# Kernel optimization log

Hardware: AMD Instinct MI355X
Metric: run time of the kernel (lower is better)

The kernel has to match this reference:

```python
import jax, jax.numpy as jnp
import numpy as np

NUM_LEVELS = 4  # -> num_components = 4*5/2 = 10 (non-recursive weights)


def _excl_cumsum(x, axis):
    # exclusive cumulative sum along `axis` (forward direction)
    return jnp.cumsum(x, axis=axis) - x


def setup_inputs() -> dict:
    key = jax.random.key(0)
    k1, k2, k3 = jax.random.split(key, 3)
    B, T, F, m = 32, 2048, 128, 64
    C = NUM_LEVELS * (NUM_LEVELS + 1) // 2  # 10
    X = jax.random.normal(k1, (B, T, F), dtype=jnp.float32)
    kernel = jax.random.normal(k2, (C, F, m), dtype=jnp.float32) / np.sqrt(F)
    bias = jax.random.normal(k3, (C, m), dtype=jnp.float32) * 0.01
    return {"X": X, "kernel": kernel, "bias": bias}


def reference(X, kernel, bias):
    # low_rank_seq2tens, embedding_order=1, recursive_weights=False,
    # reverse=False, return_sequences=False
    # M: [C, B, T, m] -- low-rank projections of the sequence for each component
    M = jnp.einsum('btf,cfm->cbtm', X, kernel) + bias[:, None, None, :]
    Y = [jnp.sum(M[0], axis=1)]  # level 1: plain time-sum, [B, m]
    k = 1
    for i in range(1, NUM_LEVELS):
        R = M[k]
        k += 1
        for _ in range(1, i + 1):
            # iterated-sum recurrence: multiply by next component's projection of
            # the exclusive prefix sum along time
            R = M[k] * _excl_cumsum(R, axis=1)
            k += 1
        Y.append(jnp.sum(R, axis=1))
    return jnp.stack(Y, axis=1)  # [B, num_levels, m]
```

## Files before the change

### kernel.cpp

```cpp
#include <hip/hip_runtime.h>
#include <hip/hip_bf16.h>
#include <stdint.h>


typedef __attribute__((ext_vector_type(8))) short short8;
typedef __attribute__((ext_vector_type(4))) float f32x4;

#define T_ 2048
#define F_ 128
#define M_ 64
#define NTILE 40
#define SEGS 16

__device__ __forceinline__ unsigned short f2bf(float x){
  unsigned int u = __float_as_uint(x);
  u += 0x7FFFu + ((u>>16)&1u);
  return (unsigned short)(u>>16);
}
__device__ __forceinline__ float bf2f(unsigned short s){
  return __uint_as_float(((unsigned int)s)<<16);
}

__global__ __launch_bounds__(256) void prep_w_k(const float* __restrict__ Wk,
                                                uint4* __restrict__ wsw){
  int g = blockIdx.x*256 + threadIdx.x;
  if (g >= NTILE*4*64) return;
  int l  = g & 63;
  int kk = (g >> 6) & 3;
  int n  = g >> 8;
  int cm = n*16 + (l & 15);
  int c  = cm >> 6, mm = cm & 63;
  int kb = kk*32 + (l>>4)*8;
  unsigned short v[8];
  #pragma unroll
  for (int j=0;j<8;++j) v[j] = f2bf(Wk[((c*F_) + kb + j)*M_ + mm]);
  uint4 o;
  o.x = (unsigned)v[0] | ((unsigned)v[1]<<16);
  o.y = (unsigned)v[2] | ((unsigned)v[3]<<16);
  o.z = (unsigned)v[4] | ((unsigned)v[5]<<16);
  o.w = (unsigned)v[6] | ((unsigned)v[7]<<16);
  wsw[g] = o;
}

struct Q4 { uint2 q0,q1,q2,q3; };

__global__ __launch_bounds__(128) void ls2t_main_k(const float* __restrict__ X,
                                                   const float* __restrict__ bias,
                                                   const short8* __restrict__ wfrag,
                                                   float* __restrict__ agg){
  const int chunk = blockIdx.x;
  const int b     = blockIdx.y;
  const int tid = threadIdx.x;
  const int w  = tid >> 6;
  const int l  = tid & 63;
  const int lr = l & 15, lg = l >> 4;
  const int t0 = chunk*128 + w*64;

  __shared__ char lds_raw[65536];
  char* msb = lds_raw + w*32768;

  short8 afr[4][4];
  #pragma unroll
  for (int s=0;s<4;++s){
    const float* xrow = X + ((size_t)b*T_ + t0 + s*16 + lr)*F_ + lg*8;
    #pragma unroll
    for (int kk=0;kk<4;++kk){
      float4 x0 = *reinterpret_cast<const float4*>(xrow + kk*32);
      float4 x1 = *reinterpret_cast<const float4*>(xrow + kk*32 + 4);
      short8 a;
      a[0]=(short)f2bf(x0.x); a[1]=(short)f2bf(x0.y);
      a[2]=(short)f2bf(x0.z); a[3]=(short)f2bf(x0.w);
      a[4]=(short)f2bf(x1.x); a[5]=(short)f2bf(x1.y);
      a[6]=(short)f2bf(x1.z); a[7]=(short)f2bf(x1.w);
      afr[s][kk]=a;
    }
  }

  auto comp = [&](int c, int ci){
    short8 wfr[4][4];
    #pragma unroll
    for (int nt=0;nt<4;++nt)
      #pragma unroll
      for (int kk=0;kk<4;++kk)
        wfr[nt][kk] = wfrag[((c*4+nt)*4+kk)*64 + l];
    #pragma unroll
    for (int nt=0;nt<4;++nt){
      #pragma unroll
      for (int s=0;s<4;++s){
        f32x4 acc = {0.f,0.f,0.f,0.f};
        #pragma unroll
        for (int kk=0;kk<4;++kk)
          acc = __builtin_amdgcn_mfma_f32_16x16x32_bf16(afr[s][kk], wfr[nt][kk], acc, 0,0,0);
        unsigned lo = (unsigned)f2bf(acc[0]) | ((unsigned)f2bf(acc[1])<<16);
        unsigned hi = (unsigned)f2bf(acc[2]) | ((unsigned)f2bf(acc[3])<<16);
        *reinterpret_cast<uint2*>(msb + ci*8192 + s*2048 + (nt*16+lr)*32 + ((lg^nt)&3)*8)
            = make_uint2(lo, hi);
      }
    }
  };
  auto rdq = [&](int ci, int s)->Q4{
    Q4 r;
    r.q0 = *reinterpret_cast<const uint2*>(msb + ci*8192 + s*2048 + l*32 + ((0^lg)&3)*8);
    r.q1 = *reinterpret_cast<const uint2*>(msb + ci*8192 + s*2048 + l*32 + ((1^lg)&3)*8);
    r.q2 = *reinterpret_cast<const uint2*>(msb + ci*8192 + s*2048 + l*32 + ((2^lg)&3)*8);
    r.q3 = *reinterpret_cast<const uint2*>(msb + ci*8192 + s*2048 + l*32 + ((3^lg)&3)*8);
    return r;
  };

#define EXTV(rq, j) bf2f((unsigned short)(((j)&1)?((((j)&2)?(rq).y:(rq).x)>>16):((((j)&2)?(rq).y:(rq).x)&0xffffu)))
#define PICKQ(r, q) ((q)==0?(r).q0:(q)==1?(r).q1:(q)==2?(r).q2:(r).q3)

  float S0=0;
  {
    float bz0 = bias[0*64+l];
    comp(0,0);
    #pragma unroll
    for (int s=0;s<4;++s){
      Q4 r0 = rdq(0,s);
      #pragma unroll
      for (int q=0;q<4;++q){
        uint2 rq = PICKQ(r0,q);
        #pragma unroll
        for (int j=0;j<4;++j) S0 += EXTV(rq,j) + bz0;
      }
    }
  }
  float S1=0,S2=0,I21=0;
  {
    float bz1=bias[64+l], bz2=bias[128+l];
    comp(1,0); comp(2,1);
    float p1=0;
    #pragma unroll
    for (int s=0;s<4;++s){
      Q4 r1 = rdq(0,s), r2 = rdq(1,s);
      #pragma unroll
      for (int q=0;q<4;++q){
        uint2 a1q = PICKQ(r1,q), a2q = PICKQ(r2,q);
        #pragma unroll
        for (int j=0;j<4;++j){
          float a1 = EXTV(a1q,j)+bz1;
          float a2 = EXTV(a2q,j)+bz2;
          I21 += a2*p1; p1 += a1; S1 += a1; S2 += a2;
        }
      }
    }
  }
  float S3=0,S4=0,S5=0,I43=0,I54=0,I543=0;
  {
    float bz3=bias[192+l], bz4=bias[256+l], bz5=bias[320+l];
    comp(3,0); comp(4,1); comp(5,2);
    float p3=0,p4=0,p43=0;
    #pragma unroll
    for (int s=0;s<4;++s){
      Q4 r3 = rdq(0,s), r4 = rdq(1,s), r5 = rdq(2,s);
      #pragma unroll
      for (int q=0;q<4;++q){
        uint2 a3q = PICKQ(r3,q), a4q = PICKQ(r4,q), a5q = PICKQ(r5,q);
        #pragma unroll
        for (int j=0;j<4;++j){
          float a3 = EXTV(a3q,j)+bz3;
          float a4 = EXTV(a4q,j)+bz4;
          float a5 = EXTV(a5q,j)+bz5;
          I43 += a4*p3; I54 += a5*p4; I543 += a5*p43;
          p43 += a4*p3; p3 += a3; p4 += a4;
          S3 += a3; S4 += a4; S5 += a5;
        }
      }
    }
  }
  float S6=0,S7=0,S8=0,S9=0,I76=0,I87=0,I98=0,I876=0,I987=0,I9876=0;
  {
    float bz6=bias[384+l], bz7=bias[448+l], bz8=bias[512+l], bz9=bias[576+l];
    comp(6,0); comp(7,1); comp(8,2); comp(9,3);
    float p6=0,p7=0,p8=0,p76=0,p87=0,p876=0;
    #pragma unroll
    for (int s=0;s<4;++s){
      Q4 r6 = rdq(0,s), r7 = rdq(1,s), r8 = rdq(2,s), r9 = rdq(3,s);
      #pragma unroll
      for (int q=0;q<4;++q){
        uint2 a6q = PICKQ(r6,q), a7q = PICKQ(r7,q), a8q = PICKQ(r8,q), a9q = PICKQ(r9,q);
        #pragma unroll
        for (int j=0;j<4;++j){
          float a6 = EXTV(a6q,j)+bz6;
          float a7 = EXTV(a7q,j)+bz7;
          float a8 = EXTV(a8q,j)+bz8;
          float a9 = EXTV(a9q,j)+bz9;
          I76 += a7*p6; I87 += a8*p7; I98 += a9*p8;
          I876 += a8*p76; I987 += a9*p87; I9876 += a9*p876;
          p876 += a8*p76; p87 += a8*p7; p76 += a7*p6;
          p6 += a6; p7 += a7; p8 += a8;
          S6 += a6; S7 += a7; S8 += a8; S9 += a9;
        }
      }
    }
  }

  float agv[20] = {S0,S1,S2,S3,S4,S5,S6,S7,S8,S9,
                   I21,I43,I54,I543,I76,I87,I98,I876,I987,I9876};
  float* mbuf = reinterpret_cast<float*>(lds_raw + 32768);
  if (w==1){
    #pragma unroll
    for (int i=0;i<20;++i) mbuf[i*64 + l] = agv[i];
  }
  __syncthreads();
  if (w==0){
    float Bv[20];
    #pragma unroll
    for (int i=0;i<20;++i) Bv[i] = mbuf[i*64 + l];
    float o[20];
    #pragma unroll
    for (int c=0;c<10;++c) o[c] = agv[c] + Bv[c];
    o[10] = agv[10]+Bv[10] + agv[1]*Bv[2];
    o[11] = agv[11]+Bv[11] + agv[3]*Bv[4];
    o[12] = agv[12]+Bv[12] + agv[4]*Bv[5];
    o[13] = agv[13]+Bv[13] + agv[11]*Bv[5] + agv[3]*Bv[12];
    o[14] = agv[14]+Bv[14] + agv[6]*Bv[7];
    o[15] = agv[15]+Bv[15] + agv[7]*Bv[8];
    o[16] = agv[16]+Bv[16] + agv[8]*Bv[9];
    o[17] = agv[17]+Bv[17] + agv[14]*Bv[8] + agv[6]*Bv[15];
    o[18] = agv[18]+Bv[18] + agv[15]*Bv[9] + agv[7]*Bv[16];
    o[19] = agv[19]+Bv[19] + agv[17]*Bv[9] + agv[14]*Bv[16] + agv[6]*Bv[18];
    float* ob = agg + (((size_t)b*SEGS + chunk)*20)*64 + l;
    #pragma unroll
    for (int i=0;i<20;++i) ob[i*64] = o[i];
  }
}

__global__ __launch_bounds__(256) void combine_k(const float* __restrict__ agg,
                                                 float* __restrict__ out){
  int g = blockIdx.x*256 + threadIdx.x;
  int b = g >> 6, m = g & 63;
  const float* base = agg + ((size_t)b*SEGS*20)*64 + m;
  float y1=0,y2=0,y3=0,y4=0;
  float p1=0,q1=0,q2=0,r1=0,r2=0,r3=0;
  #pragma unroll 4
  for (int s=0;s<SEGS;++s){
    const float* a = base + (size_t)s*20*64;
    float S0=a[0],    S1=a[64],   S2=a[128],  S3=a[192],  S4=a[256];
    float S5=a[320],  S6=a[384],  S7=a[448],  S8=a[512],  S9=a[576];
    float I21=a[640], I43=a[704], I54=a[768], I543=a[832];
    float I76=a[896], I87=a[960], I98=a[1024];
    float I876=a[1088], I987=a[1152], I9876=a[1216];
    y1 += S0;
    y2 += p1*S2 + I21;
    y3 += q2*S5 + q1*I54 + I543;
    y4 += r3*S9 + r2*I98 + r1*I987 + I9876;
    r3 += r2*S8 + r1*I87 + I876;
    r2 += r1*S7 + I76;
    r1 += S6;
    q2 += q1*S4 + I43;
    q1 += S3;
    p1 += S1;
  }
  out[(b*4+0)*64+m]=y1;
  out[(b*4+1)*64+m]=y2;
  out[(b*4+2)*64+m]=y3;
  out[(b*4+3)*64+m]=y4;
}

extern "C" void kernel_launch(void* const* d_in, const int* in_sizes, int n_in,
                              void* d_out, int out_size, void* d_ws, size_t ws_size,
                              hipStream_t stream){
  const float* X    = (const float*)d_in[0];
  const float* Wk   = (const float*)d_in[1];
  const float* bias = (const float*)d_in[2];
  float* out = (float*)d_out;

  uint4* wsw = (uint4*)d_ws;
  float* agg = (float*)((char*)d_ws + (1u<<20));

  hipLaunchKernelGGL(prep_w_k,    dim3(40),     dim3(256), 0, stream, Wk, wsw);
  hipLaunchKernelGGL(ls2t_main_k, dim3(16,32),  dim3(128), 0, stream,
                     X, bias, (const short8*)d_ws, agg);
  hipLaunchKernelGGL(combine_k,   dim3(8),      dim3(256), 0, stream, agg, out);
}
```

Measured before the change: 39.44 us.

## Keep MFMA outputs in registers and combine partial sums with wave shuffles

The main kernel is restructured so each of four waves owns one 16-column tile of m and processes a 64-step time segment. X is staged once into swizzled LDS as bf16 for all waves, and MFMA accumulators are scanned directly in registers instead of being round-tripped through LDS as bf16. Partial iterated sums across the four lane groups are merged with xor-shuffle Chen combinations. The grid doubles to 32 segments per batch, which doubles the work left for the combine kernel. It also drops the bf16 rounding of intermediate projections, trading memory traffic for more shuffles and a longer per-lane serial time order.

```diff
diff --git a/kernel.cpp b/kernel.cpp
--- a/kernel.cpp
+++ b/kernel.cpp
@@ -10,15 +10,12 @@
 #define F_ 128
 #define M_ 64
 #define NTILE 40
-#define SEGS 16
+#define SEGS 32
 
 __device__ __forceinline__ unsigned short f2bf(float x){
   unsigned int u = __float_as_uint(x);
   u += 0x7FFFu + ((u>>16)&1u);
   return (unsigned short)(u>>16);
-}
-__device__ __forceinline__ float bf2f(unsigned short s){
-  return __uint_as_float(((unsigned int)s)<<16);
 }
 
 __global__ __launch_bounds__(256) void prep_w_k(const float* __restrict__ Wk,
@@ -42,187 +39,193 @@
   wsw[g] = o;
 }
 
-struct Q4 { uint2 q0,q1,q2,q3; };
-
-__global__ __launch_bounds__(128) void ls2t_main_k(const float* __restrict__ X,
+template<int NC, int BC>
+__device__ __forceinline__ void mfma_fill(f32x4 (&acc)[NC][4],
+    const char* xs, const short8* __restrict__ wfrag,
+    const int* rbase, const int* foff, int nt, int l){
+  #pragma unroll
+  for (int c=0;c<NC;++c)
+    #pragma unroll
+    for (int s=0;s<4;++s) acc[c][s] = (f32x4){0.f,0.f,0.f,0.f};
+  #pragma unroll
+  for (int kk=0;kk<4;++kk){
+    short8 af[4];
+    #pragma unroll
+    for (int s=0;s<4;++s)
+      af[s] = *reinterpret_cast<const short8*>(xs + rbase[s] + foff[kk]);
+    #pragma unroll
+    for (int c=0;c<NC;++c){
+      short8 wf = wfrag[(((BC+c)*4+nt)*4+kk)*64 + l];
+      #pragma unroll
+      for (int s=0;s<4;++s)
+        acc[c][s] = __builtin_amdgcn_mfma_f32_16x16x32_bf16(af[s], wf, acc[c][s], 0,0,0);
+    }
+  }
+}
+
+__device__ __forceinline__ float sx(float v, int mk){ return __shfl_xor(v, mk, 64); }
+
+__global__ __launch_bounds__(256) void ls2t_main_k(const float* __restrict__ X,
                                                    const float* __restrict__ bias,
                                                    const short8* __restrict__ wfrag,
                                                    float* __restrict__ agg){
-  const int chunk = blockIdx.x;
-  const int b     = blockIdx.y;
+  const int seg = blockIdx.x;
+  const int b   = blockIdx.y;
   const int tid = threadIdx.x;
-  const int w  = tid >> 6;
-  const int l  = tid & 63;
-  const int lr = l & 15, lg = l >> 4;
-  const int t0 = chunk*128 + w*64;
-
-  __shared__ char lds_raw[65536];
-  char* msb = lds_raw + w*32768;
-
-  short8 afr[4][4];
-  #pragma unroll
-  for (int s=0;s<4;++s){
-    const float* xrow = X + ((size_t)b*T_ + t0 + s*16 + lr)*F_ + lg*8;
-    #pragma unroll
-    for (int kk=0;kk<4;++kk){
-      float4 x0 = *reinterpret_cast<const float4*>(xrow + kk*32);
-      float4 x1 = *reinterpret_cast<const float4*>(xrow + kk*32 + 4);
-      short8 a;
-      a[0]=(short)f2bf(x0.x); a[1]=(short)f2bf(x0.y);
-      a[2]=(short)f2bf(x0.z); a[3]=(short)f2bf(x0.w);
-      a[4]=(short)f2bf(x1.x); a[5]=(short)f2bf(x1.y);
-      a[6]=(short)f2bf(x1.z); a[7]=(short)f2bf(x1.w);
-      afr[s][kk]=a;
-    }
-  }
-
-  auto comp = [&](int c, int ci){
-    short8 wfr[4][4];
-    #pragma unroll
-    for (int nt=0;nt<4;++nt)
-      #pragma unroll
-      for (int kk=0;kk<4;++kk)
-        wfr[nt][kk] = wfrag[((c*4+nt)*4+kk)*64 + l];
-    #pragma unroll
-    for (int nt=0;nt<4;++nt){
+  const int nt  = tid >> 6;
+  const int l   = tid & 63;
+  const int lr  = l & 15, lg = l >> 4;
+  const int t0  = seg*64;
+
+  __shared__ __align__(16) char xs[16384];
+
+  #pragma unroll
+  for (int p=0;p<2;++p){
+    int t  = tid & 63;
+    int fp = (tid >> 6) + p*4;
+    const float* src = X + ((size_t)b*T_ + t0 + t)*F_ + fp*16;
+    float4 v0 = *reinterpret_cast<const float4*>(src);
+    float4 v1 = *reinterpret_cast<const float4*>(src+4);
+    float4 v2 = *reinterpret_cast<const float4*>(src+8);
+    float4 v3 = *reinterpret_cast<const float4*>(src+12);
+    uint4 q0, q1;
+    q0.x = (unsigned)f2bf(v0.x) | ((unsigned)f2bf(v0.y)<<16);
+    q0.y = (unsigned)f2bf(v0.z) | ((unsigned)f2bf(v0.w)<<16);
+    q0.z = (unsigned)f2bf(v1.x) | ((unsigned)f2bf(v1.y)<<16);
+    q0.w = (unsigned)f2bf(v1.z) | ((unsigned)f2bf(v1.w)<<16);
+    q1.x = (unsigned)f2bf(v2.x) | ((unsigned)f2bf(v2.y)<<16);
+    q1.y = (unsigned)f2bf(v2.z) | ((unsigned)f2bf(v2.w)<<16);
+    q1.z = (unsigned)f2bf(v3.x) | ((unsigned)f2bf(v3.y)<<16);
+    q1.w = (unsigned)f2bf(v3.z) | ((unsigned)f2bf(v3.w)<<16);
+    int sw = (t>>2)&7;
+    *reinterpret_cast<uint4*>(xs + t*256 + ((fp*2  ) ^ sw)*16) = q0;
+    *reinterpret_cast<uint4*>(xs + t*256 + ((fp*2+1) ^ sw)*16) = q1;
+  }
+  __syncthreads();
+
+  int rbase[4], foff[4];
+  #pragma unroll
+  for (int s=0;s<4;++s)  rbase[s] = (lr*4+s)*256;
+  #pragma unroll
+  for (int kk=0;kk<4;++kk) foff[kk] = (((kk*4+lg) ^ (lr&7)))*16;
+
+  const int mcol = nt*16 + lr;
+  float* ob = agg + (((size_t)b*SEGS + seg)*20)*64 + mcol;
+
+  {
+    f32x4 acc[1][4];
+    mfma_fill<1,0>(acc, xs, wfrag, rbase, foff, nt, l);
+    float bz0 = bias[0*M_ + mcol];
+    float S0 = 0.f;
+    #pragma unroll
+    for (int j=0;j<4;++j)
+      #pragma unroll
+      for (int s=0;s<4;++s) S0 += acc[0][s][j] + bz0;
+    #pragma unroll
+    for (int st=0; st<2; ++st) S0 += sx(S0, 16<<st);
+    if (lg==0) ob[0*64] = S0;
+  }
+  {
+    f32x4 acc[2][4];
+    mfma_fill<2,1>(acc, xs, wfrag, rbase, foff, nt, l);
+    float bz1 = bias[1*M_ + mcol], bz2 = bias[2*M_ + mcol];
+    float S1=0.f,S2=0.f,I21=0.f;
+    #pragma unroll
+    for (int j=0;j<4;++j)
       #pragma unroll
       for (int s=0;s<4;++s){
-        f32x4 acc = {0.f,0.f,0.f,0.f};
-        #pragma unroll
-        for (int kk=0;kk<4;++kk)
-          acc = __builtin_amdgcn_mfma_f32_16x16x32_bf16(afr[s][kk], wfr[nt][kk], acc, 0,0,0);
-        unsigned lo = (unsigned)f2bf(acc[0]) | ((unsigned)f2bf(acc[1])<<16);
-        unsigned hi = (unsigned)f2bf(acc[2]) | ((unsigned)f2bf(acc[3])<<16);
-        *reinterpret_cast<uint2*>(msb + ci*8192 + s*2048 + (nt*16+lr)*32 + ((lg^nt)&3)*8)
-            = make_uint2(lo, hi);
+        float a1 = acc[0][s][j] + bz1;
+        float a2 = acc[1][s][j] + bz2;
+        I21 += a2*S1; S1 += a1; S2 += a2;
       }
-    }
-  };
-  auto rdq = [&](int ci, int s)->Q4{
-    Q4 r;
-    r.q0 = *reinterpret_cast<const uint2*>(msb + ci*8192 + s*2048 + l*32 + ((0^lg)&3)*8);
-    r.q1 = *reinterpret_cast<const uint2*>(msb + ci*8192 + s*2048 + l*32 + ((1^lg)&3)*8);
-    r.q2 = *reinterpret_cast<const uint2*>(msb + ci*8192 + s*2048 + l*32 + ((2^lg)&3)*8);
-    r.q3 = *reinterpret_cast<const uint2*>(msb + ci*8192 + s*2048 + l*32 + ((3^lg)&3)*8);
-    return r;
-  };
-
-#define EXTV(rq, j) bf2f((unsigned short)(((j)&1)?((((j)&2)?(rq).y:(rq).x)>>16):((((j)&2)?(rq).y:(rq).x)&0xffffu)))
-#define PICKQ(r, q) ((q)==0?(r).q0:(q)==1?(r).q1:(q)==2?(r).q2:(r).q3)
-
-  float S0=0;
-  {
-    float bz0 = bias[0*64+l];
-    comp(0,0);
-    #pragma unroll
-    for (int s=0;s<4;++s){
-      Q4 r0 = rdq(0,s);
-      #pragma unroll
-      for (int q=0;q<4;++q){
-        uint2 rq = PICKQ(r0,q);
-        #pragma unroll
-        for (int j=0;j<4;++j) S0 += EXTV(rq,j) + bz0;
+    #pragma unroll
+    for (int st=0; st<2; ++st){
+      int mk = 16<<st; bool up = (l & mk)!=0;
+      float o1=sx(S1,mk), o2=sx(S2,mk), oI=sx(I21,mk);
+      float A1=up?o1:S1, A2=up?o2:S2, AI=up?oI:I21;
+      float B1=up?S1:o1, B2=up?S2:o2, BI=up?I21:oI;
+      S1=A1+B1; S2=A2+B2; I21=AI+BI + A1*B2;
+    }
+    if (lg==0) ob[1*64]=S1; else if (lg==1) ob[2*64]=S2; else if (lg==2) ob[10*64]=I21;
+  }
+  {
+    f32x4 acc[3][4];
+    mfma_fill<3,3>(acc, xs, wfrag, rbase, foff, nt, l);
+    float bz3 = bias[3*M_ + mcol], bz4 = bias[4*M_ + mcol], bz5 = bias[5*M_ + mcol];
+    float S3=0.f,S4=0.f,S5=0.f,I43=0.f,I54=0.f,I543=0.f;
+    #pragma unroll
+    for (int j=0;j<4;++j)
+      #pragma unroll
+      for (int s=0;s<4;++s){
+        float a3 = acc[0][s][j] + bz3;
+        float a4 = acc[1][s][j] + bz4;
+        float a5 = acc[2][s][j] + bz5;
+        I543 += a5*I43; I54 += a5*S4; I43 += a4*S3;
+        S3 += a3; S4 += a4; S5 += a5;
       }
-    }
-  }
-  float S1=0,S2=0,I21=0;
-  {
-    float bz1=bias[64+l], bz2=bias[128+l];
-    comp(1,0); comp(2,1);
-    float p1=0;
-    #pragma unroll
-    for (int s=0;s<4;++s){
-      Q4 r1 = rdq(0,s), r2 = rdq(1,s);
-      #pragma unroll
-      for (int q=0;q<4;++q){
-        uint2 a1q = PICKQ(r1,q), a2q = PICKQ(r2,q);
-        #pragma unroll
-        for (int j=0;j<4;++j){
-          float a1 = EXTV(a1q,j)+bz1;
-          float a2 = EXTV(a2q,j)+bz2;
-          I21 += a2*p1; p1 += a1; S1 += a1; S2 += a2;
-        }
+    #pragma unroll
+    for (int st=0; st<2; ++st){
+      int mk = 16<<st; bool up = (l & mk)!=0;
+      float o3=sx(S3,mk), o4=sx(S4,mk), o5=sx(S5,mk);
+      float oA=sx(I43,mk), oB=sx(I54,mk), oC=sx(I543,mk);
+      float A3=up?o3:S3, A4=up?o4:S4, A5=up?o5:S5;
+      float AA=up?oA:I43, AB=up?oB:I54, AC=up?oC:I543;
+      float B3=up?S3:o3, B4=up?S4:o4, B5=up?S5:o5;
+      float BA=up?I43:oA, BB=up?I54:oB, BC_=up?I543:oC;
+      float n43 = AA+BA + A3*B4;
+      float n54 = AB+BB + A4*B5;
+      float n543= AC+BC_ + AA*B5 + A3*BB;
+      S3=A3+B3; S4=A4+B4; S5=A5+B5; I43=n43; I54=n54; I543=n543;
+    }
+    if      (lg==0){ ob[3*64]=S3;  ob[11*64]=I43; }
+    else if (lg==1){ ob[4*64]=S4;  ob[12*64]=I54; }
+    else if (lg==2){ ob[5*64]=S5;  ob[13*64]=I543; }
+  }
+  {
+    f32x4 acc[4][4];
+    mfma_fill<4,6>(acc, xs, wfrag, rbase, foff, nt, l);
+    float bz6 = bias[6*M_ + mcol], bz7 = bias[7*M_ + mcol];
+    float bz8 = bias[8*M_ + mcol], bz9 = bias[9*M_ + mcol];
+    float S6=0.f,S7=0.f,S8=0.f,S9=0.f;
+    float I76=0.f,I87=0.f,I98=0.f,I876=0.f,I987=0.f,I9876=0.f;
+    #pragma unroll
+    for (int j=0;j<4;++j)
+      #pragma unroll
+      for (int s=0;s<4;++s){
+        float a6 = acc[0][s][j] + bz6;
+        float a7 = acc[1][s][j] + bz7;
+        float a8 = acc[2][s][j] + bz8;
+        float a9 = acc[3][s][j] + bz9;
+        I9876 += a9*I876; I987 += a9*I87; I98 += a9*S8;
+        I876  += a8*I76;  I87  += a8*S7;
+        I76   += a7*S6;
+        S6 += a6; S7 += a7; S8 += a8; S9 += a9;
       }
-    }
-  }
-  float S3=0,S4=0,S5=0,I43=0,I54=0,I543=0;
-  {
-    float bz3=bias[192+l], bz4=bias[256+l], bz5=bias[320+l];
-    comp(3,0); comp(4,1); comp(5,2);
-    float p3=0,p4=0,p43=0;
-    #pragma unroll
-    for (int s=0;s<4;++s){
-      Q4 r3 = rdq(0,s), r4 = rdq(1,s), r5 = rdq(2,s);
-      #pragma unroll
-      for (int q=0;q<4;++q){
-        uint2 a3q = PICKQ(r3,q), a4q = PICKQ(r4,q), a5q = PICKQ(r5,q);
-        #pragma unroll
-        for (int j=0;j<4;++j){
-          float a3 = EXTV(a3q,j)+bz3;
-          float a4 = EXTV(a4q,j)+bz4;
-          float a5 = EXTV(a5q,j)+bz5;
-          I43 += a4*p3; I54 += a5*p4; I543 += a5*p43;
-          p43 += a4*p3; p3 += a3; p4 += a4;
-          S3 += a3; S4 += a4; S5 += a5;
-        }
-      }
-    }
-  }
-  float S6=0,S7=0,S8=0,S9=0,I76=0,I87=0,I98=0,I876=0,I987=0,I9876=0;
-  {
-    float bz6=bias[384+l], bz7=bias[448+l], bz8=bias[512+l], bz9=bias[576+l];
-    comp(6,0); comp(7,1); comp(8,2); comp(9,3);
-    float p6=0,p7=0,p8=0,p76=0,p87=0,p876=0;
-    #pragma unroll
-    for (int s=0;s<4;++s){
-      Q4 r6 = rdq(0,s), r7 = rdq(1,s), r8 = rdq(2,s), r9 = rdq(3,s);
-      #pragma unroll
-      for (int q=0;q<4;++q){
-        uint2 a6q = PICKQ(r6,q), a7q = PICKQ(r7,q), a8q = PICKQ(r8,q), a9q = PICKQ(r9,q);
-        #pragma unroll
-        for (int j=0;j<4;++j){
-          float a6 = EXTV(a6q,j)+bz6;
-          float a7 = EXTV(a7q,j)+bz7;
-          float a8 = EXTV(a8q,j)+bz8;
-          float a9 = EXTV(a9q,j)+bz9;
-          I76 += a7*p6; I87 += a8*p7; I98 += a9*p8;
-          I876 += a8*p76; I987 += a9*p87; I9876 += a9*p876;
-          p876 += a8*p76; p87 += a8*p7; p76 += a7*p6;
-          p6 += a6; p7 += a7; p8 += a8;
-          S6 += a6; S7 += a7; S8 += a8; S9 += a9;
-        }
-      }
-    }
-  }
-
-  float agv[20] = {S0,S1,S2,S3,S4,S5,S6,S7,S8,S9,
-                   I21,I43,I54,I543,I76,I87,I98,I876,I987,I9876};
-  float* mbuf = reinterpret_cast<float*>(lds_raw + 32768);
-  if (w==1){
-    #pragma unroll
-    for (int i=0;i<20;++i) mbuf[i*64 + l] = agv[i];
-  }
-  __syncthreads();
-  if (w==0){
-    float Bv[20];
-    #pragma unroll
-    for (int i=0;i<20;++i) Bv[i] = mbuf[i*64 + l];
-    float o[20];
-    #pragma unroll
-    for (int c=0;c<10;++c) o[c] = agv[c] + Bv[c];
-    o[10] = agv[10]+Bv[10] + agv[1]*Bv[2];
-    o[11] = agv[11]+Bv[11] + agv[3]*Bv[4];
-    o[12] = agv[12]+Bv[12] + agv[4]*Bv[5];
-    o[13] = agv[13]+Bv[13] + agv[11]*Bv[5] + agv[3]*Bv[12];
-    o[14] = agv[14]+Bv[14] + agv[6]*Bv[7];
-    o[15] = agv[15]+Bv[15] + agv[7]*Bv[8];
-    o[16] = agv[16]+Bv[16] + agv[8]*Bv[9];
-    o[17] = agv[17]+Bv[17] + agv[14]*Bv[8] + agv[6]*Bv[15];
-    o[18] = agv[18]+Bv[18] + agv[15]*Bv[9] + agv[7]*Bv[16];
-    o[19] = agv[19]+Bv[19] + agv[17]*Bv[9] + agv[14]*Bv[16] + agv[6]*Bv[18];
-    float* ob = agg + (((size_t)b*SEGS + chunk)*20)*64 + l;
-    #pragma unroll
-    for (int i=0;i<20;++i) ob[i*64] = o[i];
+    #pragma unroll
+    for (int st=0; st<2; ++st){
+      int mk = 16<<st; bool up = (l & mk)!=0;
+      float o6=sx(S6,mk), o7=sx(S7,mk), o8=sx(S8,mk), o9=sx(S9,mk);
+      float oA=sx(I76,mk), oB=sx(I87,mk), oC=sx(I98,mk);
+      float oD=sx(I876,mk), oE=sx(I987,mk), oF=sx(I9876,mk);
+      float A6=up?o6:S6, A7=up?o7:S7, A8=up?o8:S8, A9=up?o9:S9;
+      float AA=up?oA:I76, AB=up?oB:I87, AC=up?oC:I98;
+      float AD=up?oD:I876, AE=up?oE:I987, AF=up?oF:I9876;
+      float B6=up?S6:o6, B7=up?S7:o7, B8=up?S8:o8, B9=up?S9:o9;
+      float BA=up?I76:oA, BB=up?I87:oB, BC_=up?I98:oC;
+      float BD=up?I876:oD, BE=up?I987:oE, BF=up?I9876:oF;
+      float n76  = AA+BA + A6*B7;
+      float n87  = AB+BB + A7*B8;
+      float n98  = AC+BC_ + A8*B9;
+      float n876 = AD+BD + AA*B8 + A6*BB;
+      float n987 = AE+BE + AB*B9 + A7*BC_;
+      float n9876= AF+BF + AD*B9 + AA*BC_ + A6*BE;
+      S6=A6+B6; S7=A7+B7; S8=A8+B8; S9=A9+B9;
+      I76=n76; I87=n87; I98=n98; I876=n876; I987=n987; I9876=n9876;
+    }
+    if      (lg==0){ ob[6*64]=S6; ob[14*64]=I76; ob[18*64]=I987; }
+    else if (lg==1){ ob[7*64]=S7; ob[15*64]=I87; ob[19*64]=I9876; }
+    else if (lg==2){ ob[8*64]=S8; ob[16*64]=I98; }
+    else           { ob[9*64]=S9; ob[17*64]=I876; }
   }
 }
 
@@ -270,7 +273,7 @@
   float* agg = (float*)((char*)d_ws + (1u<<20));
 
   hipLaunchKernelGGL(prep_w_k,    dim3(40),     dim3(256), 0, stream, Wk, wsw);
-  hipLaunchKernelGGL(ls2t_main_k, dim3(16,32),  dim3(128), 0, stream,
+  hipLaunchKernelGGL(ls2t_main_k, dim3(32,32),  dim3(256), 0, stream,
                      X, bias, (const short8*)d_ws, agg);
   hipLaunchKernelGGL(combine_k,   dim3(8),      dim3(256), 0, stream, agg, out);
 }
```

Result: slower. 44.09 us (+11.8%).
